# Kernel optimization log

Measured on AMD Instinct MI355X. Metric: run time of the kernel, lower is better.

## Reference

```python
import jax, jax.numpy as jnp
import numpy as np

N_NODES = 50000


def _gcn(x, row, col, w, b, n):
    # add self loops
    loops = jnp.arange(n, dtype=row.dtype)
    row = jnp.concatenate([row, loops])
    col = jnp.concatenate([col, loops])
    h = x @ w  # [N, out]
    deg = jax.ops.segment_sum(jnp.ones(col.shape, h.dtype), col, num_segments=n)
    dinv = jnp.where(deg > 0, deg ** -0.5, 0.0)
    norm = dinv[row] * dinv[col]  # [E+N]
    msg = norm[:, None] * h[row]
    out = jax.ops.segment_sum(msg, col, num_segments=n)
    return out + b


def _edgeconv(x, row, col, w1, b1, w2, b2, n):
    x_i = x[col]            # target features
    x_j = x[row]            # source features
    t = jnp.concatenate([x_i, x_j - x_i], axis=1)  # [E, 2*hidden]
    m = jax.nn.relu(t @ w1 + b1) @ w2 + b2          # [E, hidden]
    agg = jax.ops.segment_max(m, col, num_segments=n)
    # PyG fills empty segments with 0, segment_max fills with -inf
    return jnp.where(jnp.isfinite(agg), agg, 0.0)


def setup_inputs() -> dict:
    key = jax.random.key(0)
    ks = jax.random.split(key, 10)
    n, e = N_NODES, 800000
    cin, ch, cout = 32, 64, 16
    x = jax.random.normal(ks[0], (n, cin), dtype=jnp.float32)
    edge_index = jax.random.randint(ks[1], (2, e), 0, n, dtype=jnp.int64)

    def glorot(k, shape):
        lim = (6.0 / (shape[0] + shape[1])) ** 0.5
        return jax.random.uniform(k, shape, jnp.float32, -lim, lim)

    return {
        "x": x,
        "edge_index": edge_index,
        "gcn1_w": glorot(ks[2], (cin, ch)),
        "gcn1_b": jnp.zeros((ch,), jnp.float32),
        "edge_w1": glorot(ks[3], (2 * ch, ch)),
        "edge_b1": jnp.zeros((ch,), jnp.float32),
        "edge_w2": glorot(ks[4], (ch, ch)),
        "edge_b2": jnp.zeros((ch,), jnp.float32),
        "gcn2_w": glorot(ks[5], (ch, cout)),
        "gcn2_b": jnp.zeros((cout,), jnp.float32),
    }


def reference(x, edge_index, gcn1_w, gcn1_b, edge_w1, edge_b1, edge_w2, edge_b2, gcn2_w, gcn2_b):
    n = x.shape[0]
    row, col = edge_index[0], edge_index[1]
    h = jnp.tanh(_gcn(x, row, col, gcn1_w, gcn1_b, n))
    h = jax.nn.relu(_edgeconv(h, row, col, edge_w1, edge_b1, edge_w2, edge_b2, n))
    out = _gcn(h, row, col, gcn2_w, gcn2_b, n)
    return out
```

## Files before the change

kernel.cpp:

```cpp
#include <hip/hip_runtime.h>


typedef __attribute__((ext_vector_type(8))) short short8;
typedef __attribute__((ext_vector_type(4))) float f32x4;
typedef __attribute__((ext_vector_type(8))) _Float16 f16x8;
typedef __attribute__((ext_vector_type(4))) _Float16 f16x4;
typedef __attribute__((ext_vector_type(2))) _Float16 f16x2;

#define FILL_CH 4096

__device__ __forceinline__ unsigned short f2bf(float x) {
    unsigned int u = __float_as_uint(x);
    return (unsigned short)((u + 0x7FFFu + ((u >> 16) & 1u)) >> 16);
}
__device__ __forceinline__ float bf2f(unsigned short h) {
    return __uint_as_float(((unsigned int)h) << 16);
}
__device__ __forceinline__ void splitT(float u, short& hi, short& lo) {
    unsigned int ub = __float_as_uint(u);
    hi = (short)(ub >> 16);
    float r = u - __uint_as_float(ub & 0xFFFF0000u);
    lo = (short)(__float_as_uint(r) >> 16);
}
__device__ __forceinline__ f16x8 relu8(f16x8 v) {
    f16x8 z = {0, 0, 0, 0, 0, 0, 0, 0};
#if __has_builtin(__builtin_elementwise_max)
    return __builtin_elementwise_max(v, z);
#else
    f16x8 o;
#pragma unroll
    for (int j = 0; j < 8; ++j) o[j] = v[j] > (_Float16)0 ? v[j] : (_Float16)0;
    return o;
#endif
}

#define ROR_ADD(s, CTRL)                                                         \
    s += __int_as_float(__builtin_amdgcn_update_dpp(                             \
        0, __float_as_int(s), (CTRL), 0xf, 0xf, false))
#define ROR8_ADD(s) ROR_ADD(s, 0x128)

__global__ __launch_bounds__(256) void k_fill_a(
        const int* __restrict__ row, const int* __restrict__ col,
        const float4* __restrict__ x4, f16x4* __restrict__ xh4,
        int* __restrict__ bcnt, int* __restrict__ stage, int E, int m4, int nb) {
    __shared__ int cnt[512];
    __shared__ int base[512];
    int tid = threadIdx.x;
    int nth = gridDim.x * 256;
    for (int idx = blockIdx.x * 256 + tid; idx < m4; idx += nth) {
        float4 v = x4[idx];
        f16x4 o;
        o[0] = (_Float16)v.x; o[1] = (_Float16)v.y;
        o[2] = (_Float16)v.z; o[3] = (_Float16)v.w;
        xh4[idx] = o;
    }
    for (int i = tid; i < nb; i += 256) cnt[i] = 0;
    __syncthreads();
    int e0 = blockIdx.x * FILL_CH;
    int r[16], c[16];
#pragma unroll
    for (int i = 0; i < 16; ++i) {
        int e = e0 + tid + i * 256;
        if (e < E) {
            r[i] = row[e]; c[i] = col[e];
            atomicAdd(&cnt[c[i] >> 7], 1);
        } else c[i] = -1;
    }
    __syncthreads();
    for (int i = tid; i < nb; i += 256)
        base[i] = cnt[i] ? (i << 12) + atomicAdd(&bcnt[i], cnt[i]) : 0;
    __syncthreads();
    for (int i = tid; i < nb; i += 256) cnt[i] = 0;
    __syncthreads();
#pragma unroll
    for (int i = 0; i < 16; ++i) {
        if (c[i] >= 0) {
            int b = c[i] >> 7;
            int lp = atomicAdd(&cnt[b], 1);
            stage[base[b] + lp] = (r[i] << 7) | (c[i] & 127);
        }
    }
}

__global__ __launch_bounds__(256) void k_fill_b2(
        const int* __restrict__ bcnt, const int* __restrict__ stage,
        int* __restrict__ ptr, float* __restrict__ dinv, int* __restrict__ csr,
        int n, int nb, int E) {
    __shared__ int lcnt[128];
    __shared__ int lcur[128];
    __shared__ int wtotS;
    __shared__ int wsum[4];
    __shared__ int gbaseS;
    int b = blockIdx.x, tid = threadIdx.x;
    int lane = tid & 63, w = tid >> 6;
    int c0 = b << 7;
    int s0 = b << 12;
    int tot = bcnt[b];
    if (tid < 128) lcnt[tid] = 0;
    int acc = 0;
    if (tid < b && tid < nb) acc += bcnt[tid];
    int t2 = tid + 256;
    if (t2 < b && t2 < nb) acc += bcnt[t2];
#pragma unroll
    for (int off = 1; off < 64; off <<= 1) acc += __shfl_xor(acc, off);
    if (lane == 0) wsum[w] = acc;
    __syncthreads();
    if (tid == 0) {
        gbaseS = wsum[0] + wsum[1] + wsum[2] + wsum[3];
        if (b == nb - 1) ptr[n] = E;
    }
    for (int p = tid; p < tot; p += 256)
        atomicAdd(&lcnt[stage[s0 + p] & 127], 1);
    __syncthreads();
    int gbase = gbaseS;
    int v = (tid < 128) ? lcnt[tid] : 0;
    int s = v;
    for (int off = 1; off < 64; off <<= 1) {
        int t = __shfl_up(s, off, 64);
        if (lane >= off) s += t;
    }
    if (tid == 63) wtotS = s;
    __syncthreads();
    int excl = s - v + ((w == 1) ? wtotS : 0);
    if (tid < 128) {
        int c = c0 + tid;
        int basep = gbase + excl;
        lcur[tid] = basep;
        if (c < n) {
            ptr[c] = basep;
            dinv[c] = rsqrtf((float)(v + 1));
        }
    }
    __syncthreads();
    for (int p = tid; p < tot; p += 256) {
        int vv = stage[s0 + p];
        int pos = atomicAdd(&lcur[vv & 127], 1);
        csr[pos] = vv >> 7;
    }
}

__global__ __launch_bounds__(256) void k_gather32(
        const int* __restrict__ ptr, const int* __restrict__ csr_row,
        const float* __restrict__ x, const _Float16* __restrict__ xh,
        const float* __restrict__ dinv, float* __restrict__ agg, int n) {
    int wid = blockIdx.x * 4 + (threadIdx.x >> 6);
    if (wid >= n) return;
    int lane = threadIdx.x & 63;
    int f4 = lane & 7, slot = lane >> 3;
    int v = wid;
    int start = ptr[v], end = ptr[v + 1];
    const f16x4* xh4 = (const f16x4*)xh;
    float sx = 0.f, sy = 0.f, sz = 0.f, sw = 0.f;
    int p = start + slot;
    int r = (p < end) ? csr_row[p] : 0;
    while (p < end) {
        int rcur = r;
        int pn = p + 8;
        if (pn < end) r = csr_row[pn];
        float dr = dinv[rcur];
        f16x4 xv = xh4[(size_t)rcur * 8 + f4];
        sx = fmaf(dr, (float)xv[0], sx);
        sy = fmaf(dr, (float)xv[1], sy);
        sz = fmaf(dr, (float)xv[2], sz);
        sw = fmaf(dr, (float)xv[3], sw);
        p = pn;
    }
    ROR8_ADD(sx); ROR8_ADD(sy); ROR8_ADD(sz); ROR8_ADD(sw);
#pragma unroll
    for (int off = 16; off < 64; off <<= 1) {
        sx += __shfl_xor(sx, off); sy += __shfl_xor(sy, off);
        sz += __shfl_xor(sz, off); sw += __shfl_xor(sw, off);
    }
    if (slot == 0) {
        float dv = dinv[v], d2 = dv * dv;
        float4 xv = ((const float4*)x)[(size_t)v * 8 + f4];
        float4 o;
        o.x = dv * sx + d2 * xv.x;
        o.y = dv * sy + d2 * xv.y;
        o.z = dv * sz + d2 * xv.z;
        o.w = dv * sw + d2 * xv.w;
        ((float4*)agg)[(size_t)v * 8 + f4] = o;
    }
}

__global__ __launch_bounds__(256, 1) void k_h1tab(
        const float* __restrict__ agg, const float* __restrict__ gw,
        const float* __restrict__ gb, const float* __restrict__ w1,
        const float* __restrict__ b1,
        _Float16* __restrict__ atab, _Float16* __restrict__ btab, int ntiles) {
    __shared__ float tileS[4][16 * 66];
    int lane = threadIdx.x & 63;
    int wv = threadIdx.x >> 6;
    int n16 = lane & 15, q = lane >> 4;
    float* T = tileS[wv];

    short8 gh[4], gl[4];
    float gbias[4];
#pragma unroll
    for (int t = 0; t < 4; ++t) {
        gbias[t] = gb[t * 16 + n16];
        short8 hh, ll;
#pragma unroll
        for (int j = 0; j < 8; ++j) {
            float w = gw[(q * 8 + j) * 64 + t * 16 + n16];
            unsigned short wh = f2bf(w);
            hh[j] = (short)wh;
            ll[j] = (short)f2bf(w - bf2f(wh));
        }
        gh[t] = hh; gl[t] = ll;
    }
    short8 th[4][2], tl[4][2], uh[4][2], ul[4][2];
    float bias1[4];
#pragma unroll
    for (int t = 0; t < 4; ++t) {
        bias1[t] = b1[t * 16 + n16];
#pragma unroll
        for (int ck = 0; ck < 2; ++ck) {
            short8 h1v, l1v, h2v, l2v;
#pragma unroll
            for (int j = 0; j < 8; ++j) {
                int d = ck * 32 + q * 8 + j;
                float wbv = w1[(64 + d) * 64 + t * 16 + n16];
                float wtv = w1[d * 64 + t * 16 + n16] - wbv;
                unsigned short x1 = f2bf(wtv);
                h1v[j] = (short)x1; l1v[j] = (short)f2bf(wtv - bf2f(x1));
                unsigned short x2 = f2bf(wbv);
                h2v[j] = (short)x2; l2v[j] = (short)f2bf(wbv - bf2f(x2));
            }
            th[t][ck] = h1v; tl[t][ck] = l1v;
            uh[t][ck] = h2v; ul[t][ck] = l2v;
        }
    }

    int nwaves = gridDim.x * 4;
    int wid = blockIdx.x * 4 + wv;
    for (int tile = wid; tile < ntiles; tile += nwaves) {
        int v0 = tile * 16;
        const float4* a4 = (const float4*)(agg + (size_t)(v0 + n16) * 32);
        float4 A0 = a4[2 * q], A1 = a4[2 * q + 1];
        float a[8] = {A0.x, A0.y, A0.z, A0.w, A1.x, A1.y, A1.z, A1.w};
        short8 ah, al;
#pragma unroll
        for (int j = 0; j < 8; ++j) { short h, l; splitT(a[j], h, l); ah[j] = h; al[j] = l; }
#pragma unroll
        for (int t = 0; t < 4; ++t) {
            f32x4 acc = (f32x4){gbias[t], gbias[t], gbias[t], gbias[t]};
            acc = __builtin_amdgcn_mfma_f32_16x16x32_bf16(ah, gh[t], acc, 0, 0, 0);
            acc = __builtin_amdgcn_mfma_f32_16x16x32_bf16(al, gh[t], acc, 0, 0, 0);
            acc = __builtin_amdgcn_mfma_f32_16x16x32_bf16(ah, gl[t], acc, 0, 0, 0);
#pragma unroll
            for (int i = 0; i < 4; ++i)
                T[(q * 4 + i) * 66 + t * 16 + n16] = tanhf(acc[i]);
        }
        float b[16];
#pragma unroll
        for (int j = 0; j < 8; ++j) {
            b[j]     = T[n16 * 66 + q * 8 + j];
            b[8 + j] = T[n16 * 66 + 32 + q * 8 + j];
        }
        short8 ah0, ah1, al0, al1;
#pragma unroll
        for (int j = 0; j < 8; ++j) {
            short h, l;
            splitT(b[j], h, l);      ah0[j] = h; al0[j] = l;
            splitT(b[8 + j], h, l);  ah1[j] = h; al1[j] = l;
        }
#pragma unroll
        for (int t = 0; t < 4; ++t) {
            f32x4 aa = (f32x4){bias1[t], bias1[t], bias1[t], bias1[t]};
            aa = __builtin_amdgcn_mfma_f32_16x16x32_bf16(ah0, th[t][0], aa, 0, 0, 0);
            aa = __builtin_amdgcn_mfma_f32_16x16x32_bf16(ah1, th[t][1], aa, 0, 0, 0);
            aa = __builtin_amdgcn_mfma_f32_16x16x32_bf16(al0, th[t][0], aa, 0, 0, 0);
            aa = __builtin_amdgcn_mfma_f32_16x16x32_bf16(al1, th[t][1], aa, 0, 0, 0);
            aa = __builtin_amdgcn_mfma_f32_16x16x32_bf16(ah0, tl[t][0], aa, 0, 0, 0);
            aa = __builtin_amdgcn_mfma_f32_16x16x32_bf16(ah1, tl[t][1], aa, 0, 0, 0);
            f32x4 bb = (f32x4){0.f, 0.f, 0.f, 0.f};
            bb = __builtin_amdgcn_mfma_f32_16x16x32_bf16(ah0, uh[t][0], bb, 0, 0, 0);
            bb = __builtin_amdgcn_mfma_f32_16x16x32_bf16(ah1, uh[t][1], bb, 0, 0, 0);
            bb = __builtin_amdgcn_mfma_f32_16x16x32_bf16(al0, uh[t][0], bb, 0, 0, 0);
            bb = __builtin_amdgcn_mfma_f32_16x16x32_bf16(al1, uh[t][1], bb, 0, 0, 0);
            bb = __builtin_amdgcn_mfma_f32_16x16x32_bf16(ah0, ul[t][0], bb, 0, 0, 0);
            bb = __builtin_amdgcn_mfma_f32_16x16x32_bf16(ah1, ul[t][1], bb, 0, 0, 0);
#pragma unroll
            for (int i = 0; i < 4; ++i) {
                size_t off = (size_t)(v0 + q * 4 + i) * 64 + t * 16 + n16;
                atab[off] = (_Float16)aa[i];
                btab[off] = (_Float16)bb[i];
            }
        }
    }
}

__global__ __launch_bounds__(256) void k_edge_mlp(
        const int* __restrict__ ptr, const int* __restrict__ csr_row,
        const _Float16* __restrict__ atab, const _Float16* __restrict__ btab,
        const float* __restrict__ w2, const float* __restrict__ b2,
        const float* __restrict__ wg, _Float16* __restrict__ h2h, int n) {
    int lane = threadIdx.x & 63;
    int n16 = lane & 15, q = lane >> 4;

    f16x8 wh[4][2];
    float bias[4];
    float wgf[4][4];
#pragma unroll
    for (int t = 0; t < 4; ++t) {
        bias[t] = b2[t * 16 + n16];
#pragma unroll
        for (int jj = 0; jj < 4; ++jj)
            wgf[t][jj] = wg[(t * 16 + n16) * 16 + q * 4 + jj];
#pragma unroll
        for (int ck = 0; ck < 2; ++ck) {
            f16x8 hh;
#pragma unroll
            for (int j = 0; j < 8; ++j)
                hh[j] = (_Float16)w2[(ck * 32 + q * 8 + j) * 64 + t * 16 + n16];
            wh[t][ck] = hh;
        }
    }
    const f32x4 z4 = (f32x4){0.f, 0.f, 0.f, 0.f};

    int nwaves = gridDim.x * 4;
    int wid = blockIdx.x * 4 + (threadIdx.x >> 6);
    if (wid >= n) return;

    int c = wid;
    int st = ptr[c], ed = ptr[c + 1];
    {
        int deg = ed - st;
        int nf = deg >> 4, rm = deg & 15;
        int rrem0 = (rm > 0 && n16 < rm) ? csr_row[st + (nf << 4) + n16] : 0;
        int r0 = (nf > 0) ? csr_row[st + n16] : 0;
        int r = r0, rrem = rrem0;
        while (true) {
            int cn = c + nwaves;
            bool hasN = cn < n;
            int stn = 0, edn = 0;
            if (hasN) { stn = ptr[cn]; edn = ptr[cn + 1]; }

            const f16x8* a8 = (const f16x8*)(atab + (size_t)c * 64);
            f16x8 A0 = a8[q], A1 = a8[4 + q];
            float red[4] = {0.f, 0.f, 0.f, 0.f};

            int deg2 = ed - st;
            int nfull = deg2 >> 4;
            int rem = deg2 & 15;
            for (int ft = 0; ft < nfull; ++ft) {
                int rcur = r;
                if (ft + 1 < nfull) r = csr_row[st + (ft + 1) * 16 + n16];
                const f16x8* b8 = (const f16x8*)(btab + (size_t)rcur * 64);
                f16x8 u0 = relu8(A0 + b8[q]);
                f16x8 u1 = relu8(A1 + b8[4 + q]);
                __builtin_amdgcn_s_setprio(1);
#pragma unroll
                for (int t = 0; t < 4; ++t) {
                    f32x4 a = __builtin_amdgcn_mfma_f32_16x16x32_f16(u0, wh[t][0], z4, 0, 0, 0);
                    a = __builtin_amdgcn_mfma_f32_16x16x32_f16(u1, wh[t][1], a, 0, 0, 0);
                    float mx = fmaxf(fmaxf(a[0], a[1]), fmaxf(a[2], a[3]));
                    red[t] = fmaxf(red[t], mx + bias[t]);
                }
                __builtin_amdgcn_s_setprio(0);
            }
            if (rem > 0) {
                f16x8 u0 = {0, 0, 0, 0, 0, 0, 0, 0};
                f16x8 u1 = {0, 0, 0, 0, 0, 0, 0, 0};
                if (n16 < rem) {
                    const f16x8* b8 = (const f16x8*)(btab + (size_t)rrem * 64);
                    u0 = relu8(A0 + b8[q]);
                    u1 = relu8(A1 + b8[4 + q]);
                }
                __builtin_amdgcn_s_setprio(1);
#pragma unroll
                for (int t = 0; t < 4; ++t) {
                    f32x4 a = __builtin_amdgcn_mfma_f32_16x16x32_f16(u0, wh[t][0], z4, 0, 0, 0);
                    a = __builtin_amdgcn_mfma_f32_16x16x32_f16(u1, wh[t][1], a, 0, 0, 0);
#pragma unroll
                    for (int i = 0; i < 4; ++i)
                        if (q * 4 + i < rem) red[t] = fmaxf(red[t], a[i] + bias[t]);
                }
                __builtin_amdgcn_s_setprio(0);
            }

            int rn = 0, rremn = 0;
            if (hasN) {
                int degn = edn - stn;
                int nfn = degn >> 4, rmn = degn & 15;
                if (rmn > 0 && n16 < rmn) rremn = csr_row[stn + (nfn << 4) + n16];
                if (nfn > 0) rn = csr_row[stn + n16];
            }

#pragma unroll
            for (int t = 0; t < 4; ++t) {
                red[t] = fmaxf(red[t], __shfl_xor(red[t], 16));
                red[t] = fmaxf(red[t], __shfl_xor(red[t], 32));
            }
            float part[4];
#pragma unroll
            for (int jj = 0; jj < 4; ++jj) {
                part[jj] = red[0] * wgf[0][jj];
                part[jj] = fmaf(red[1], wgf[1][jj], part[jj]);
                part[jj] = fmaf(red[2], wgf[2][jj], part[jj]);
                part[jj] = fmaf(red[3], wgf[3][jj], part[jj]);
                ROR_ADD(part[jj], 0x121);
                ROR_ADD(part[jj], 0x122);
                ROR_ADD(part[jj], 0x124);
                ROR_ADD(part[jj], 0x128);
            }
            if (n16 == 0) {
                f16x4 ph;
                ph[0] = (_Float16)part[0]; ph[1] = (_Float16)part[1];
                ph[2] = (_Float16)part[2]; ph[3] = (_Float16)part[3];
                ((f16x4*)(h2h + (size_t)c * 16))[q] = ph;
            }

            if (!hasN) break;
            c = cn; st = stn; ed = edn; r = rn; rrem = rremn;
        }
    }
}

__global__ __launch_bounds__(256) void k_gcn2_gather(
        const int* __restrict__ ptr, const int* __restrict__ csr_row,
        const _Float16* __restrict__ h2h, const float* __restrict__ dinv,
        const float* __restrict__ bg, float* __restrict__ out, int n) {
    int wid = blockIdx.x * 4 + (threadIdx.x >> 6);
    if (wid >= n) return;
    int lane = threadIdx.x & 63;
    int f2 = lane & 7, slot = lane >> 3;
    int c = wid;
    int start = ptr[c], end = ptr[c + 1];
    const f16x2* h22 = (const f16x2*)h2h;
    float sx = 0.f, sy = 0.f;
    int p = start + slot;
    int r = (p < end) ? csr_row[p] : 0;
    while (p < end) {
        int rcur = r;
        int pn = p + 8;
        if (pn < end) r = csr_row[pn];
        float dr = dinv[rcur];
        f16x2 hv = h22[(size_t)rcur * 8 + f2];
        sx = fmaf(dr, (float)hv[0], sx);
        sy = fmaf(dr, (float)hv[1], sy);
        p = pn;
    }
    ROR8_ADD(sx); ROR8_ADD(sy);
#pragma unroll
    for (int off = 16; off < 64; off <<= 1) {
        sx += __shfl_xor(sx, off);
        sy += __shfl_xor(sy, off);
    }
    if (slot == 0) {
        float dv = dinv[c];
        f16x2 hv = h22[(size_t)c * 8 + f2];
        float2 o;
        o.x = bg[2 * f2]     + dv * (dv * (float)hv[0] + sx);
        o.y = bg[2 * f2 + 1] + dv * (dv * (float)hv[1] + sy);
        ((float2*)out)[(size_t)c * 8 + f2] = o;
    }
}

extern "C" void kernel_launch(void* const* d_in, const int* in_sizes, int n_in,
                              void* d_out, int out_size, void* d_ws, size_t ws_size,
                              hipStream_t stream) {
    const float* x   = (const float*)d_in[0];
    const int*   ei  = (const int*)d_in[1];
    const float* g1w = (const float*)d_in[2];
    const float* g1b = (const float*)d_in[3];
    const float* ew1 = (const float*)d_in[4];
    const float* eb1 = (const float*)d_in[5];
    const float* ew2 = (const float*)d_in[6];
    const float* eb2 = (const float*)d_in[7];
    const float* g2w = (const float*)d_in[8];
    const float* g2b = (const float*)d_in[9];
    float* out = (float*)d_out;
    float* ws  = (float*)d_ws;

    const int n = in_sizes[0] / 32;
    const int E = in_sizes[1] / 2;
    const int* row = ei;
    const int* col = ei + E;
    const int ntiles = (n + 15) / 16;
    const int nbuck = (n + 127) >> 7;

    size_t npad    = ((size_t)n + 63) & ~(size_t)63;
    size_t o_misc  = 0;
    size_t o_ptr   = 1024;
    size_t o_csr   = o_ptr + npad + 64;
    size_t o_dinv  = o_csr + (size_t)E;
    size_t o_atab  = o_dinv + npad;
    size_t o_btab  = o_atab + (size_t)n * 32;
    size_t o_agg   = o_btab + (size_t)n * 32;
    size_t o_xh    = o_agg + (size_t)n * 32;
    size_t o_h2h   = o_xh + (size_t)n * 16;
    size_t o_stage = o_h2h + (size_t)n * 8;

    int*      bcnt   = (int*)(ws + o_misc);
    int*      ptr    = (int*)(ws + o_ptr);
    int*      csr    = (int*)(ws + o_csr);
    float*    dinv   = ws + o_dinv;
    _Float16* atab   = (_Float16*)(ws + o_atab);
    _Float16* btab   = (_Float16*)(ws + o_btab);
    float*    agg    = ws + o_agg;
    _Float16* xh     = (_Float16*)(ws + o_xh);
    _Float16* h2h    = (_Float16*)(ws + o_h2h);
    int*      stage  = (int*)(ws + o_stage);

    int nblk = (n + 3) / 4;
    int fill_nb = (E + FILL_CH - 1) / FILL_CH;
    int m4 = n * 8;

    hipMemsetAsync(bcnt, 0, 512 * sizeof(int), stream);
    k_fill_a<<<fill_nb, 256, 0, stream>>>(row, col, (const float4*)x, (f16x4*)xh,
                                          bcnt, stage, E, m4, nbuck);
    k_fill_b2<<<nbuck, 256, 0, stream>>>(bcnt, stage, ptr, dinv, csr, n, nbuck, E);
    k_gather32<<<nblk, 256, 0, stream>>>(ptr, csr, x, xh, dinv, agg, n);
    k_h1tab<<<256, 256, 0, stream>>>(agg, g1w, g1b, ew1, eb1, atab, btab, ntiles);
    k_edge_mlp<<<2048, 256, 0, stream>>>(ptr, csr, atab, btab, ew2, eb2, g2w, h2h, n);
    k_gcn2_gather<<<nblk, 256, 0, stream>>>(ptr, csr, h2h, dinv, g2b, out, n);
}
```

Baseline: 187.2 us.

## Make GCN gathers persistent with next-node prefetch; drop counter reset in fill

The two GCN gather kernels now run as persistent grid-stride loops over 2048 blocks. Each wave prefetches the next node's CSR range and first neighbour index while it finishes reducing and storing the current node, hiding that pointer-chasing latency. In k_fill_a the second shared counter pass and its extra barrier are replaced by atomics directly on the per-bucket base offsets. Fewer waves per node means less launch and tail parallelism, and there is some extra register pressure.

```diff
diff --git a/kernel.cpp b/kernel.cpp
--- a/kernel.cpp
+++ b/kernel.cpp
@@ -70,14 +70,12 @@
     for (int i = tid; i < nb; i += 256)
         base[i] = cnt[i] ? (i << 12) + atomicAdd(&bcnt[i], cnt[i]) : 0;
     __syncthreads();
-    for (int i = tid; i < nb; i += 256) cnt[i] = 0;
-    __syncthreads();
 #pragma unroll
     for (int i = 0; i < 16; ++i) {
         if (c[i] >= 0) {
             int b = c[i] >> 7;
-            int lp = atomicAdd(&cnt[b], 1);
-            stage[base[b] + lp] = (r[i] << 7) | (c[i] & 127);
+            int lp = atomicAdd(&base[b], 1);
+            stage[lp] = (r[i] << 7) | (c[i] & 127);
         }
     }
 }
@@ -143,43 +141,59 @@
         const int* __restrict__ ptr, const int* __restrict__ csr_row,
         const float* __restrict__ x, const _Float16* __restrict__ xh,
         const float* __restrict__ dinv, float* __restrict__ agg, int n) {
+    int lane = threadIdx.x & 63;
+    int f4 = lane & 7, slot = lane >> 3;
+    const f16x4* xh4 = (const f16x4*)xh;
+
+    int nwaves = gridDim.x * 4;
     int wid = blockIdx.x * 4 + (threadIdx.x >> 6);
     if (wid >= n) return;
-    int lane = threadIdx.x & 63;
-    int f4 = lane & 7, slot = lane >> 3;
-    int v = wid;
-    int start = ptr[v], end = ptr[v + 1];
-    const f16x4* xh4 = (const f16x4*)xh;
-    float sx = 0.f, sy = 0.f, sz = 0.f, sw = 0.f;
-    int p = start + slot;
-    int r = (p < end) ? csr_row[p] : 0;
-    while (p < end) {
-        int rcur = r;
-        int pn = p + 8;
-        if (pn < end) r = csr_row[pn];
-        float dr = dinv[rcur];
-        f16x4 xv = xh4[(size_t)rcur * 8 + f4];
-        sx = fmaf(dr, (float)xv[0], sx);
-        sy = fmaf(dr, (float)xv[1], sy);
-        sz = fmaf(dr, (float)xv[2], sz);
-        sw = fmaf(dr, (float)xv[3], sw);
-        p = pn;
-    }
-    ROR8_ADD(sx); ROR8_ADD(sy); ROR8_ADD(sz); ROR8_ADD(sw);
-#pragma unroll
-    for (int off = 16; off < 64; off <<= 1) {
-        sx += __shfl_xor(sx, off); sy += __shfl_xor(sy, off);
-        sz += __shfl_xor(sz, off); sw += __shfl_xor(sw, off);
-    }
-    if (slot == 0) {
-        float dv = dinv[v], d2 = dv * dv;
-        float4 xv = ((const float4*)x)[(size_t)v * 8 + f4];
-        float4 o;
-        o.x = dv * sx + d2 * xv.x;
-        o.y = dv * sy + d2 * xv.y;
-        o.z = dv * sz + d2 * xv.z;
-        o.w = dv * sw + d2 * xv.w;
-        ((float4*)agg)[(size_t)v * 8 + f4] = o;
+
+    int c = wid;
+    int st = ptr[c], ed = ptr[c + 1];
+    int r0 = (st + slot < ed) ? csr_row[st + slot] : 0;
+    while (true) {
+        int cn = c + nwaves;
+        bool hasN = cn < n;
+        int stn = 0, edn = 0;
+        if (hasN) { stn = ptr[cn]; edn = ptr[cn + 1]; }
+
+        float sx = 0.f, sy = 0.f, sz = 0.f, sw = 0.f;
+        int p = st + slot;
+        int r = r0;
+        while (p < ed) {
+            int rcur = r;
+            int pn = p + 8;
+            if (pn < ed) r = csr_row[pn];
+            float dr = dinv[rcur];
+            f16x4 xv = xh4[(size_t)rcur * 8 + f4];
+            sx = fmaf(dr, (float)xv[0], sx);
+            sy = fmaf(dr, (float)xv[1], sy);
+            sz = fmaf(dr, (float)xv[2], sz);
+            sw = fmaf(dr, (float)xv[3], sw);
+            p = pn;
+        }
+        int r0n = 0;
+        if (hasN && stn + slot < edn) r0n = csr_row[stn + slot];
+
+        ROR8_ADD(sx); ROR8_ADD(sy); ROR8_ADD(sz); ROR8_ADD(sw);
+#pragma unroll
+        for (int off = 16; off < 64; off <<= 1) {
+            sx += __shfl_xor(sx, off); sy += __shfl_xor(sy, off);
+            sz += __shfl_xor(sz, off); sw += __shfl_xor(sw, off);
+        }
+        if (slot == 0) {
+            float dv = dinv[c], d2 = dv * dv;
+            float4 xv = ((const float4*)x)[(size_t)c * 8 + f4];
+            float4 o;
+            o.x = dv * sx + d2 * xv.x;
+            o.y = dv * sy + d2 * xv.y;
+            o.z = dv * sz + d2 * xv.z;
+            o.w = dv * sw + d2 * xv.w;
+            ((float4*)agg)[(size_t)c * 8 + f4] = o;
+        }
+        if (!hasN) break;
+        c = cn; st = stn; ed = edn; r0 = r0n;
     }
 }
 
@@ -422,39 +436,55 @@
         const int* __restrict__ ptr, const int* __restrict__ csr_row,
         const _Float16* __restrict__ h2h, const float* __restrict__ dinv,
         const float* __restrict__ bg, float* __restrict__ out, int n) {
+    int lane = threadIdx.x & 63;
+    int f2 = lane & 7, slot = lane >> 3;
+    const f16x2* h22 = (const f16x2*)h2h;
+
+    int nwaves = gridDim.x * 4;
     int wid = blockIdx.x * 4 + (threadIdx.x >> 6);
     if (wid >= n) return;
-    int lane = threadIdx.x & 63;
-    int f2 = lane & 7, slot = lane >> 3;
+
     int c = wid;
-    int start = ptr[c], end = ptr[c + 1];
-    const f16x2* h22 = (const f16x2*)h2h;
-    float sx = 0.f, sy = 0.f;
-    int p = start + slot;
-    int r = (p < end) ? csr_row[p] : 0;
-    while (p < end) {
-        int rcur = r;
-        int pn = p + 8;
-        if (pn < end) r = csr_row[pn];
-        float dr = dinv[rcur];
-        f16x2 hv = h22[(size_t)rcur * 8 + f2];
-        sx = fmaf(dr, (float)hv[0], sx);
-        sy = fmaf(dr, (float)hv[1], sy);
-        p = pn;
-    }
-    ROR8_ADD(sx); ROR8_ADD(sy);
-#pragma unroll
-    for (int off = 16; off < 64; off <<= 1) {
-        sx += __shfl_xor(sx, off);
-        sy += __shfl_xor(sy, off);
-    }
-    if (slot == 0) {
-        float dv = dinv[c];
-        f16x2 hv = h22[(size_t)c * 8 + f2];
-        float2 o;
-        o.x = bg[2 * f2]     + dv * (dv * (float)hv[0] + sx);
-        o.y = bg[2 * f2 + 1] + dv * (dv * (float)hv[1] + sy);
-        ((float2*)out)[(size_t)c * 8 + f2] = o;
+    int st = ptr[c], ed = ptr[c + 1];
+    int r0 = (st + slot < ed) ? csr_row[st + slot] : 0;
+    while (true) {
+        int cn = c + nwaves;
+        bool hasN = cn < n;
+        int stn = 0, edn = 0;
+        if (hasN) { stn = ptr[cn]; edn = ptr[cn + 1]; }
+
+        float sx = 0.f, sy = 0.f;
+        int p = st + slot;
+        int r = r0;
+        while (p < ed) {
+            int rcur = r;
+            int pn = p + 8;
+            if (pn < ed) r = csr_row[pn];
+            float dr = dinv[rcur];
+            f16x2 hv = h22[(size_t)rcur * 8 + f2];
+            sx = fmaf(dr, (float)hv[0], sx);
+            sy = fmaf(dr, (float)hv[1], sy);
+            p = pn;
+        }
+        int r0n = 0;
+        if (hasN && stn + slot < edn) r0n = csr_row[stn + slot];
+
+        ROR8_ADD(sx); ROR8_ADD(sy);
+#pragma unroll
+        for (int off = 16; off < 64; off <<= 1) {
+            sx += __shfl_xor(sx, off);
+            sy += __shfl_xor(sy, off);
+        }
+        if (slot == 0) {
+            float dv = dinv[c];
+            f16x2 hv = h22[(size_t)c * 8 + f2];
+            float2 o;
+            o.x = bg[2 * f2]     + dv * (dv * (float)hv[0] + sx);
+            o.y = bg[2 * f2 + 1] + dv * (dv * (float)hv[1] + sy);
+            ((float2*)out)[(size_t)c * 8 + f2] = o;
+        }
+        if (!hasN) break;
+        c = cn; st = stn; ed = edn; r0 = r0n;
     }
 }
 
@@ -504,7 +534,6 @@
     _Float16* h2h    = (_Float16*)(ws + o_h2h);
     int*      stage  = (int*)(ws + o_stage);
 
-    int nblk = (n + 3) / 4;
     int fill_nb = (E + FILL_CH - 1) / FILL_CH;
     int m4 = n * 8;
 
@@ -512,8 +541,8 @@
     k_fill_a<<<fill_nb, 256, 0, stream>>>(row, col, (const float4*)x, (f16x4*)xh,
                                           bcnt, stage, E, m4, nbuck);
     k_fill_b2<<<nbuck, 256, 0, stream>>>(bcnt, stage, ptr, dinv, csr, n, nbuck, E);
-    k_gather32<<<nblk, 256, 0, stream>>>(ptr, csr, x, xh, dinv, agg, n);
+    k_gather32<<<2048, 256, 0, stream>>>(ptr, csr, x, xh, dinv, agg, n);
     k_h1tab<<<256, 256, 0, stream>>>(agg, g1w, g1b, ew1, eb1, atab, btab, ntiles);
     k_edge_mlp<<<2048, 256, 0, stream>>>(ptr, csr, atab, btab, ew2, eb2, g2w, h2h, n);
-    k_gcn2_gather<<<nblk, 256, 0, stream>>>(ptr, csr, h2h, dinv, g2b, out, n);
-}
+    k_gcn2_gather<<<2048, 256, 0, stream>>>(ptr, csr, h2h, dinv, g2b, out, n);
+}
```

Measured after the change: 181.5 us. 1.03x faster.
